# Performance work log

Hardware: AMD Instinct MI355X
Metric: run time of the kernel (lower is better)

## Reference

```python
import jax, jax.numpy as jnp
import numpy as np

H, W = 4096, 4096
KH, KW = 3, 3


def setup_inputs() -> dict:
    key = jax.random.key(0)
    k1, k2, k3 = jax.random.split(key, 3)
    X = jax.random.normal(k1, (H, W), dtype=jnp.float32)
    weight = jax.random.normal(k2, (KH, KW), dtype=jnp.float32)
    bias = jax.random.normal(k3, (1,), dtype=jnp.float32)
    return {"X": X, "weight": weight, "bias": bias}


def reference(X, weight, bias):
    # Valid 2D cross-correlation (no kernel flip), matching the torch double loop:
    # Y[i, j] = sum(X[i:i+h, j:j+w] * K) + bias
    lhs = X[None, None, :, :]          # NCHW
    rhs = weight[None, None, :, :]     # OIHW
    out = jax.lax.conv_general_dilated(
        lhs, rhs,
        window_strides=(1, 1),
        padding="VALID",
        dimension_numbers=("NCHW", "OIHW", "NCHW"),
    )
    return out[0, 0] + bias[0]  # [H-KH+1, W-KW+1]
```

## Files before the change

### kernel.cpp

```cpp
#include <hip/hip_runtime.h>


constexpr int Hin = 4096;
constexpr int Win = 4096;
constexpr int OH  = 4094;
constexpr int OW  = 4094;

constexpr int R = 4;

__global__ __launch_bounds__(256, 8) void conv3x3_kernel(
    const float* __restrict__ X, const float* __restrict__ Wt,
    const float* __restrict__ B, float* __restrict__ Out)
{
    int nb = gridDim.x;
    int b  = blockIdx.x;
    int b2 = (b & 7) * (nb >> 3) + (b >> 3);

    int bx   = b2 >> 10;
    int by   = b2 & 1023;
    int wave = threadIdx.x >> 6;
    int lane = threadIdx.x & 63;

    int c  = bx * 512 + wave * 128 + 2 * lane;
    int r0 = by * R;

    int v1c = (c + 2 <= Win - 2) ? (c + 2) : (Win - 2);

    float2 v0[R + 2], v1[R + 2];
#pragma unroll
    for (int ir = 0; ir < R + 2; ++ir) {
        int rr = r0 + ir;
        if (rr > Hin - 1) rr = Hin - 1;
        const float* row = X + (size_t)rr * Win;
        v0[ir] = *reinterpret_cast<const float2*>(row + c);
        v1[ir] = *reinterpret_cast<const float2*>(row + v1c);
    }

    float w[9];
#pragma unroll
    for (int i = 0; i < 9; ++i) w[i] = Wt[i];
    const float bias = B[0];

    float2 acc[R];
#pragma unroll
    for (int i = 0; i < R; ++i) { acc[i].x = bias; acc[i].y = bias; }

#pragma unroll
    for (int i = 0; i < R; ++i) {
#pragma unroll
        for (int kh = 0; kh < 3; ++kh) {
            int ir = i + kh;
            float w0 = w[kh * 3 + 0], w1 = w[kh * 3 + 1], w2 = w[kh * 3 + 2];
            acc[i].x = fmaf(v0[ir].x, w0, acc[i].x);
            acc[i].x = fmaf(v0[ir].y, w1, acc[i].x);
            acc[i].x = fmaf(v1[ir].x, w2, acc[i].x);
            acc[i].y = fmaf(v0[ir].y, w0, acc[i].y);
            acc[i].y = fmaf(v1[ir].x, w1, acc[i].y);
            acc[i].y = fmaf(v1[ir].y, w2, acc[i].y);
        }
    }

    if (c < OW) {
#pragma unroll
        for (int i = 0; i < R; ++i) {
            int orow = r0 + i;
            if (orow < OH) {
                *reinterpret_cast<float2*>(Out + (size_t)orow * OW + c) = acc[i];
            }
        }
    }
}

extern "C" void kernel_launch(void* const* d_in, const int* in_sizes, int n_in,
                              void* d_out, int out_size, void* d_ws, size_t ws_size,
                              hipStream_t stream) {
    const float* X  = (const float*)d_in[0];
    const float* Wt = (const float*)d_in[1];
    const float* B  = (const float*)d_in[2];
    float* Out      = (float*)d_out;

    int blocks = 8 * 1024;
    conv3x3_kernel<<<blocks, 256, 0, stream>>>(X, Wt, B, Out);
}
```

Baseline: 26.50 us.

## Process 16 rows per thread with sliding register window and prefetch

```diff
diff --git a/kernel.cpp b/kernel.cpp
--- a/kernel.cpp
+++ b/kernel.cpp
@@ -6,7 +6,9 @@
 constexpr int OH  = 4094;
 constexpr int OW  = 4094;
 
-constexpr int R = 4;
+constexpr int TR = 4;
+constexpr int NT = 4;
+constexpr int BR = TR * NT;
 
 __global__ __launch_bounds__(256, 8) void conv3x3_kernel(
     const float* __restrict__ X, const float* __restrict__ Wt,
@@ -16,57 +18,79 @@
     int b  = blockIdx.x;
     int b2 = (b & 7) * (nb >> 3) + (b >> 3);
 
-    int bx   = b2 >> 10;
-    int by   = b2 & 1023;
+    int bx   = b2 >> 8;
+    int by   = b2 & 255;
     int wave = threadIdx.x >> 6;
     int lane = threadIdx.x & 63;
 
     int c  = bx * 512 + wave * 128 + 2 * lane;
-    int r0 = by * R;
+    int r0 = by * BR;
 
     int v1c = (c + 2 <= Win - 2) ? (c + 2) : (Win - 2);
-
-    float2 v0[R + 2], v1[R + 2];
-#pragma unroll
-    for (int ir = 0; ir < R + 2; ++ir) {
-        int rr = r0 + ir;
-        if (rr > Hin - 1) rr = Hin - 1;
-        const float* row = X + (size_t)rr * Win;
-        v0[ir] = *reinterpret_cast<const float2*>(row + c);
-        v1[ir] = *reinterpret_cast<const float2*>(row + v1c);
-    }
 
     float w[9];
 #pragma unroll
     for (int i = 0; i < 9; ++i) w[i] = Wt[i];
     const float bias = B[0];
 
-    float2 acc[R];
+    float2 w0[6], w1[6];
 #pragma unroll
-    for (int i = 0; i < R; ++i) { acc[i].x = bias; acc[i].y = bias; }
+    for (int j = 0; j < 6; ++j) {
+        int rr = r0 + j;
+        if (rr > Hin - 1) rr = Hin - 1;
+        const float* row = X + (size_t)rr * Win;
+        w0[j] = *reinterpret_cast<const float2*>(row + c);
+        w1[j] = *reinterpret_cast<const float2*>(row + v1c);
+    }
 
 #pragma unroll
-    for (int i = 0; i < R; ++i) {
+    for (int t = 0; t < NT; ++t) {
+        float2 p0[TR], p1[TR];
+        if (t < NT - 1) {
 #pragma unroll
-        for (int kh = 0; kh < 3; ++kh) {
-            int ir = i + kh;
-            float w0 = w[kh * 3 + 0], w1 = w[kh * 3 + 1], w2 = w[kh * 3 + 2];
-            acc[i].x = fmaf(v0[ir].x, w0, acc[i].x);
-            acc[i].x = fmaf(v0[ir].y, w1, acc[i].x);
-            acc[i].x = fmaf(v1[ir].x, w2, acc[i].x);
-            acc[i].y = fmaf(v0[ir].y, w0, acc[i].y);
-            acc[i].y = fmaf(v1[ir].x, w1, acc[i].y);
-            acc[i].y = fmaf(v1[ir].y, w2, acc[i].y);
+            for (int j = 0; j < TR; ++j) {
+                int rr = r0 + t * TR + 6 + j;
+                if (rr > Hin - 1) rr = Hin - 1;
+                const float* row = X + (size_t)rr * Win;
+                p0[j] = *reinterpret_cast<const float2*>(row + c);
+                p1[j] = *reinterpret_cast<const float2*>(row + v1c);
+            }
         }
-    }
 
-    if (c < OW) {
+        float2 acc[TR];
 #pragma unroll
-        for (int i = 0; i < R; ++i) {
-            int orow = r0 + i;
-            if (orow < OH) {
-                *reinterpret_cast<float2*>(Out + (size_t)orow * OW + c) = acc[i];
+        for (int i = 0; i < TR; ++i) { acc[i].x = bias; acc[i].y = bias; }
+
+#pragma unroll
+        for (int i = 0; i < TR; ++i) {
+#pragma unroll
+            for (int kh = 0; kh < 3; ++kh) {
+                int ir = i + kh;
+                float q0 = w[kh * 3 + 0], q1 = w[kh * 3 + 1], q2 = w[kh * 3 + 2];
+                acc[i].x = fmaf(w0[ir].x, q0, acc[i].x);
+                acc[i].x = fmaf(w0[ir].y, q1, acc[i].x);
+                acc[i].x = fmaf(w1[ir].x, q2, acc[i].x);
+                acc[i].y = fmaf(w0[ir].y, q0, acc[i].y);
+                acc[i].y = fmaf(w1[ir].x, q1, acc[i].y);
+                acc[i].y = fmaf(w1[ir].y, q2, acc[i].y);
             }
+        }
+
+        if (c < OW) {
+#pragma unroll
+            for (int i = 0; i < TR; ++i) {
+                int orow = r0 + t * TR + i;
+                if (orow < OH) {
+                    *reinterpret_cast<float2*>(Out + (size_t)orow * OW + c) = acc[i];
+                }
+            }
+        }
+
+        if (t < NT - 1) {
+            w0[0] = w0[4]; w0[1] = w0[5];
+            w1[0] = w1[4]; w1[1] = w1[5];
+#pragma unroll
+            for (int j = 0; j < TR; ++j) { w0[2 + j] = p0[j]; w1[2 + j] = p1[j]; }
         }
     }
 }
@@ -79,6 +103,6 @@
     const float* B  = (const float*)d_in[2];
     float* Out      = (float*)d_out;
 
-    int blocks = 8 * 1024;
+    int blocks = 8 * 256;
     conv3x3_kernel<<<blocks, 256, 0, stream>>>(X, Wt, B, Out);
 }
```

After: 40.78 us. +53.9%, slower.
